# Kernel optimization log

Hardware: AMD Instinct MI355X
Metric: run time of the kernel (lower is better)

Reference implementation:

```python
import jax, jax.numpy as jnp
import numpy as np

N, L, H, E, FE = 32, 128, 16, 256, 4  # batch, seq_len, heads, embed_size, forward_expansion
EPS = 1e-5
NEG_SLOPE = 0.01


def _mask_positions(qe):
    # zero entries where j < L-1-i (torch: triu(ones,1).flip(1) == 1)
    Ld = qe.shape[-1]
    i = jnp.arange(Ld)[:, None]
    j = jnp.arange(Ld)[None, :]
    return jnp.where(j >= (Ld - 1 - i), qe, jnp.zeros((), qe.dtype))


def _skew(qe):
    # pad last dim on the left, reinterpret, drop first row -> relative skew
    n, h, Ld, _ = qe.shape
    p = jnp.pad(qe, ((0, 0), (0, 0), (0, 0), (1, 0)))
    return p.reshape(n, h, Ld + 1, Ld)[:, :, 1:, :]


def _batchnorm(x, gamma, beta):
    # BatchNorm1d(C=L*H) over (N, C, E): normalize over batch and embed dims
    mean = jnp.mean(x, axis=(0, 2), keepdims=True)
    var = jnp.var(x, axis=(0, 2), keepdims=True)
    return (x - mean) * jax.lax.rsqrt(var + EPS) * gamma[None, :, None] + beta[None, :, None]


def _leaky(x):
    return jnp.where(x >= 0, x, NEG_SLOPE * x)


def setup_inputs() -> dict:
    key = jax.random.key(0)
    ks = jax.random.split(key, 16)
    s_e = 1.0 / np.sqrt(E)
    d = {
        "x": jax.random.normal(ks[0], (N, L * H, E, 1), dtype=jnp.float32),
        "Wq": jax.random.normal(ks[1], (E, E), dtype=jnp.float32) * s_e,
        "bq": jnp.zeros((E,), jnp.float32),
        "Wk": jax.random.normal(ks[2], (E, E), dtype=jnp.float32) * s_e,
        "bk": jnp.zeros((E,), jnp.float32),
        "Wv": jax.random.normal(ks[3], (E, E), dtype=jnp.float32) * s_e,
        "bv": jnp.zeros((E,), jnp.float32),
        "Erel": jax.random.normal(ks[4], (H, L, E), dtype=jnp.float32),
        "Wo": jax.random.normal(ks[5], (E, E), dtype=jnp.float32) * s_e,
        "bo": jnp.zeros((E,), jnp.float32),
        "g1": jnp.ones((L * H,), jnp.float32),
        "be1": jnp.zeros((L * H,), jnp.float32),
        "g2": jnp.ones((L * H,), jnp.float32),
        "be2": jnp.zeros((L * H,), jnp.float32),
        "W1": jax.random.normal(ks[6], (E, FE * E), dtype=jnp.float32) * s_e,
        "b1": jnp.zeros((FE * E,), jnp.float32),
        "W2": jax.random.normal(ks[7], (FE * E, E), dtype=jnp.float32) * (1.0 / np.sqrt(FE * E)),
        "b2": jnp.zeros((E,), jnp.float32),
        "Wenc": jax.random.normal(ks[8], (E, E), dtype=jnp.float32) * s_e,
        "benc": jnp.zeros((E,), jnp.float32),
    }
    return d


def reference(x, Wq, bq, Wk, bk, Wv, bv, Erel, Wo, bo, g1, be1, g2, be2, W1, b1, W2, b2, Wenc, benc):
    xs = x[:, :, :, 0]  # (N, L*H, E)
    q = (xs @ Wq + bq).reshape(N, L, H, E)
    k = (xs @ Wk + bk).reshape(N, L, H, E)
    v = (xs @ Wv + bv).reshape(N, L, H, E)
    # relative-position skew term (Music-Transformer style)
    QE = jnp.einsum('nlhe,hme->nhlm', q, Erel)       # (N,H,L,L)
    S = _skew(_mask_positions(QE))                   # (N,H,L,L)
    qk = jnp.einsum('nqhe,nkhe->nhqk', q, k)         # (N,H,L,L)
    att = jax.nn.softmax(qk / jnp.sqrt(jnp.float32(E)), axis=-1) + S
    z = jnp.einsum('nhql,nlhe->nqhe', att, v).reshape(N, L * H, E)
    z = z @ Wo + bo
    h1 = _batchnorm(z + xs, g1, be1)
    ff = _leaky(h1 @ W1 + b1) @ W2 + b2
    out = _batchnorm(ff + h1, g2, be2)
    return out @ Wenc + benc
```

## Files before the change

kernel.cpp:

```cpp
#include <hip/hip_runtime.h>
#include <hip/hip_bf16.h>

using u16 = unsigned short;
typedef __attribute__((ext_vector_type(8))) short bf16x8;
typedef __attribute__((ext_vector_type(4))) float f32x4;

static constexpr float EPS_ = 1e-5f;
static constexpr float NEG_ = 0.01f;

__device__ __forceinline__ float bf2f(u16 u) { return __uint_as_float(((unsigned)u) << 16); }
__device__ __forceinline__ u16 f2bf(float f) {
    union { __hip_bfloat16 h; u16 u; } c; c.h = __float2bfloat16(f); return c.u;
}

#define MFMA16(a, b, c) __builtin_amdgcn_mfma_f32_16x16x32_bf16(a, b, c, 0, 0, 0)

__device__ __forceinline__ void gload16(const u16* g, u16* l) {
    __builtin_amdgcn_global_load_lds(
        (__attribute__((address_space(1))) void*)(u16*)g,
        (__attribute__((address_space(3))) void*)l, 16, 0, 0);
}

__device__ __forceinline__ void zero_acc(f32x4 acc[4][4]) {
    #pragma unroll
    for (int i = 0; i < 4; i++)
        #pragma unroll
        for (int j = 0; j < 4; j++)
            acc[i][j] = (f32x4){0.f, 0.f, 0.f, 0.f};
}

__device__ __forceinline__ int xswz(int nwg) {
    const int b = blockIdx.x;
    return (b & 7) * (nwg >> 3) + (b >> 3);
}

__device__ __forceinline__ void lds_core(
    const u16* __restrict__ Ag, int lda,
    const u16* __restrict__ Bg, int ldb, int K,
    u16* As, u16* Bs, f32x4 acc[4][4])
{
    const int tid = threadIdx.x;
    const int w = tid >> 6, lane = tid & 63;
    const int g = lane >> 4, r = lane & 15;
    const int wm = (w >> 1) * 64, wn = (w & 1) * 64;

    for (int kt = 0; kt < K; kt += 64) {
        #pragma unroll
        for (int j = 0; j < 4; j++) {
            const int ubase = (w * 4 + j) * 64;
            const int u = ubase + lane;
            const int row = u >> 3, cb = (u & 7) * 8;
            gload16(Ag + (size_t)row * lda + kt + cb, As + ubase * 8);
            gload16(Bg + (size_t)row * ldb + kt + cb, Bs + ubase * 8);
        }
        __syncthreads();
        #pragma unroll
        for (int kk = 0; kk < 2; kk++) {
            bf16x8 af[4], bfr[4];
            #pragma unroll
            for (int f = 0; f < 4; f++) {
                af[f]  = *(const bf16x8*)(As + (wm + f * 16 + r) * 64 + kk * 32 + g * 8);
                bfr[f] = *(const bf16x8*)(Bs + (wn + f * 16 + r) * 64 + kk * 32 + g * 8);
            }
            #pragma unroll
            for (int i = 0; i < 4; i++)
                #pragma unroll
                for (int j = 0; j < 4; j++)
                    acc[i][j] = MFMA16(af[i], bfr[j], acc[i][j]);
        }
        __syncthreads();
    }
}

template<int EPI, bool VTRANS, typename OutF, typename ResF>
__device__ __forceinline__ void epi_store(
    u16* Cs, f32x4 (&acc)[4][4], const float* biasBase, float scale,
    OutF outp, ResF resp)
{
    const int tid = threadIdx.x;
    const int w = tid >> 6, lane = tid & 63;
    const int g = lane >> 4, r = lane & 15;
    const int mb = (w >> 1) * 64, nb = (w & 1) * 64;

    #pragma unroll
    for (int fn = 0; fn < 4; fn++) {
        const int col = nb + fn * 16 + r;
        const float bv = biasBase ? biasBase[col] : 0.f;
        #pragma unroll
        for (int fm = 0; fm < 4; fm++) {
            #pragma unroll
            for (int reg = 0; reg < 4; reg++) {
                const int row = mb + fm * 16 + g * 4 + reg;
                float v = acc[fm][fn][reg] * scale + bv;
                if (EPI == 1) v = v >= 0.f ? v : NEG_ * v;
                int R, C;
                if (VTRANS) { R = col; C = ((row & 15) << 3) | (row >> 4); }
                else        { R = row; C = col; }
                Cs[R * 136 + C] = f2bf(v);
            }
        }
    }
    __syncthreads();
    #pragma unroll
    for (int p = 0; p < 8; p++) {
        const int ck = p * 256 + tid;
        const int row = ck >> 4, cc = ck & 15;
        bf16x8 v = *(const bf16x8*)(Cs + row * 136 + cc * 8);
        if constexpr (EPI == 3) {
            const bf16x8 rv = *(const bf16x8*)resp(row, cc);
            #pragma unroll
            for (int j = 0; j < 8; j++)
                v[j] = (short)f2bf(bf2f((u16)v[j]) + bf2f((u16)rv[j]));
        }
        *(bf16x8*)outp(row, cc) = v;
    }
}

__global__ __launch_bounds__(256) void cvt_k(const float* __restrict__ in,
                                             u16* __restrict__ out) {
    const size_t i8 = ((size_t)blockIdx.x * 256 + threadIdx.x) * 8;
    const float4 lo = *(const float4*)(in + i8);
    const float4 hi = *(const float4*)(in + i8 + 4);
    ushort4 o0, o1;
    o0.x = f2bf(lo.x); o0.y = f2bf(lo.y); o0.z = f2bf(lo.z); o0.w = f2bf(lo.w);
    o1.x = f2bf(hi.x); o1.y = f2bf(hi.y); o1.z = f2bf(hi.z); o1.w = f2bf(hi.w);
    *(ushort4*)(out + i8) = o0;
    *(ushort4*)(out + i8 + 4) = o1;
}

__global__ __launch_bounds__(256) void prep_w_k(
    const float* __restrict__ Wq, const float* __restrict__ Wk,
    const float* __restrict__ Wv, const float* __restrict__ Wo,
    const float* __restrict__ Wenc, const float* __restrict__ W1,
    const float* __restrict__ W2, const float* __restrict__ Erel,
    u16* __restrict__ Wqkvt, u16* __restrict__ Wot, u16* __restrict__ Wenct,
    u16* __restrict__ W1t, u16* __restrict__ W2t, u16* __restrict__ Erelb)
{
    const int bid = blockIdx.x, tid = threadIdx.x;
    if (bid < 1280) {
        const int jb = bid >> 8;
        const int t = ((bid & 255) << 8) | tid;
        const int n = t >> 8, k = t & 255;
        const float* src = jb == 0 ? Wq : jb == 1 ? Wk : jb == 2 ? Wv
                         : jb == 3 ? Wo : Wenc;
        const u16 v = f2bf(src[(k << 8) + n]);
        if (jb < 3)       Wqkvt[jb * 65536 + t] = v;
        else if (jb == 3) Wot[t] = v;
        else              Wenct[t] = v;
    } else if (bid < 2304) {
        const int t = ((bid - 1280) << 8) | tid;
        const int n = t >> 8, k = t & 255;
        W1t[t] = f2bf(W1[(k << 10) + n]);
    } else if (bid < 3328) {
        const int t = ((bid - 2304) << 8) | tid;
        const int n = t >> 10, k = t & 1023;
        W2t[t] = f2bf(W2[(k << 8) + n]);
    } else {
        const int t = ((bid - 3328) << 8) | tid;
        Erelb[t] = f2bf(Erel[t]);
    }
}

__global__ __launch_bounds__(256) void qkv_k(
    const u16* __restrict__ xbf, const u16* __restrict__ Wqkvt,
    const float* __restrict__ bq, const float* __restrict__ bk,
    const float* __restrict__ bv,
    u16* __restrict__ qo, u16* __restrict__ ko, u16* __restrict__ vo)
{
    __shared__ __align__(16) u16 SH[17408];
    u16* As = SH; u16* Bs = SH + 8192;
    const int f = xswz(3072);
    const int nblk = f % 6, mblk = f / 6;
    const int m0 = mblk * 128, n0 = nblk * 128;
    const int which = n0 >> 8;
    const float* bias = which == 0 ? bq : (which == 1 ? bk : bv);
    const int e0 = n0 & 255;

    f32x4 acc[4][4]; zero_acc(acc);
    lds_core(xbf + (size_t)m0 * 256, 256, Wqkvt + (size_t)n0 * 256, 256, 256,
             As, Bs, acc);

    const int nn = m0 >> 11, l0 = (m0 & 2047) >> 4;
    auto dummy = [&](int, int) -> const u16* { return nullptr; };
    if (which == 2) {
        epi_store<0, true>(SH, acc, bias + e0, 1.f,
            [&](int row, int cc) -> u16* {
                return vo + ((size_t)(nn * 16 + cc) * 256 + e0 + row) * 128 + l0;
            }, dummy);
    } else {
        u16* out = which == 0 ? qo : ko;
        epi_store<0, false>(SH, acc, bias + e0, 1.f,
            [&](int row, int cc) -> u16* {
                const int m = m0 + row;
                const int l = (m & 2047) >> 4, hh = m & 15;
                return out + ((size_t)(nn * 16 + hh) * 128 + l) * 256 + e0 + cc * 8;
            }, dummy);
    }
}

__global__ __launch_bounds__(256) void qkqe_k(
    const u16* __restrict__ q, const u16* __restrict__ kc,
    const u16* __restrict__ erel, u16* __restrict__ out)
{
    __shared__ __align__(16) u16 SH[17408];
    u16* As = SH; u16* Bs = SH + 8192;
    const int f = xswz(1024);
    const int b = f >> 1, h = b & 15;
    const int n0 = (f & 1) * 128;
    const u16* Ag = q + (size_t)b * 128 * 256;
    const u16* Bg = (n0 == 0) ? (kc + (size_t)b * 128 * 256)
                              : (erel + (size_t)h * 128 * 256);

    f32x4 acc[4][4]; zero_acc(acc);
    lds_core(Ag, 256, Bg, 256, 256, As, Bs, acc);

    const float scale = (n0 == 0) ? 0.0625f : 1.0f;
    auto dummy = [&](int, int) -> const u16* { return nullptr; };
    epi_store<0, false>(SH, acc, nullptr, scale,
        [&](int row, int cc) -> u16* {
            return out + ((size_t)b * 128 + row) * 256 + n0 + cc * 8;
        }, dummy);
}

__global__ __launch_bounds__(256) void softmax_k(
    const u16* __restrict__ qk, u16* __restrict__ att)
{
    const int r = blockIdx.x * 4 + (threadIdx.x >> 6);
    const int lane = threadIdx.x & 63;
    const int i = r & 127;
    const u16* row = qk + (size_t)r * 256;
    const float x0 = bf2f(row[lane]), x1 = bf2f(row[lane + 64]);
    float mx = fmaxf(x0, x1);
    #pragma unroll
    for (int o = 32; o; o >>= 1) mx = fmaxf(mx, __shfl_xor(mx, o));
    const float e0 = __expf(x0 - mx), e1 = __expf(x1 - mx);
    float s = e0 + e1;
    #pragma unroll
    for (int o = 32; o; o >>= 1) s += __shfl_xor(s, o);
    const float rinv = 1.0f / s;
    const float s0 = (lane <= i) ? bf2f(row[128 + 127 - i + lane]) : 0.f;
    const float s1 = (lane + 64 <= i) ? bf2f(row[128 + 127 - i + lane + 64]) : 0.f;
    att[(size_t)r * 128 + lane] = f2bf(e0 * rinv + s0);
    att[(size_t)r * 128 + lane + 64] = f2bf(e1 * rinv + s1);
}

__global__ __launch_bounds__(256) void av_k(
    const u16* __restrict__ att, const u16* __restrict__ vT,
    u16* __restrict__ zc)
{
    __shared__ __align__(16) u16 SH[17408];
    u16* As = SH; u16* Bs = SH + 8192;
    const int f = xswz(1024);
    const int b = f >> 1;
    const int n0 = (f & 1) * 128;
    const u16* Ag = att + (size_t)b * 128 * 128;
    const u16* Bg = vT + (size_t)b * 256 * 128 + (size_t)n0 * 128;

    f32x4 acc[4][4]; zero_acc(acc);
    lds_core(Ag, 128, Bg, 128, 128, As, Bs, acc);

    const int nn = b >> 4, hh = b & 15;
    auto dummy = [&](int, int) -> const u16* { return nullptr; };
    epi_store<0, false>(SH, acc, nullptr, 1.f,
        [&](int row, int cc) -> u16* {
            return zc + ((size_t)(nn * 2048 + row * 16 + hh)) * 256 + n0 + cc * 8;
        }, dummy);
}

template<int K, int Nn, int EPI, typename TO>
__global__ __launch_bounds__(256) void gemm_k(
    const u16* __restrict__ A, const u16* __restrict__ Wt,
    const float* __restrict__ bias, const u16* __restrict__ res,
    TO* __restrict__ out)
{
    __shared__ __align__(16) u16 SH[17408];
    u16* As = SH; u16* Bs = SH + 8192;
    constexpr int NB = Nn / 128;
    const int f = xswz(512 * NB);
    const int m0 = (f / NB) * 128, n0 = (f % NB) * 128;

    f32x4 acc[4][4]; zero_acc(acc);
    lds_core(A + (size_t)m0 * K, K, Wt + (size_t)n0 * K, K, K, As, Bs, acc);

    if constexpr (sizeof(TO) == 2) {
        epi_store<EPI, false>(SH, acc, bias + n0, 1.f,
            [&](int row, int cc) -> u16* {
                return ((u16*)out) + (size_t)(m0 + row) * Nn + n0 + cc * 8;
            },
            [&](int row, int cc) -> const u16* {
                return res + (size_t)(m0 + row) * Nn + n0 + cc * 8;
            });
    } else {
        const int tid = threadIdx.x;
        const int w = tid >> 6, lane = tid & 63;
        const int g = lane >> 4, r = lane & 15;
        const int mb = m0 + (w >> 1) * 64, nb = n0 + (w & 1) * 64;
        #pragma unroll
        for (int fn = 0; fn < 4; fn++) {
            const int n = nb + fn * 16 + r;
            const float bv4 = bias[n];
            #pragma unroll
            for (int fm = 0; fm < 4; fm++) {
                #pragma unroll
                for (int reg = 0; reg < 4; reg++) {
                    const int m = mb + fm * 16 + g * 4 + reg;
                    ((float*)out)[(size_t)m * Nn + n] = acc[fm][fn][reg] + bv4;
                }
            }
        }
    }
}

__global__ __launch_bounds__(256) void bnstats_k(
    const u16* __restrict__ x, const float* __restrict__ g,
    const float* __restrict__ be, float2* __restrict__ params)
{
    const int c = blockIdx.x, tid = threadIdx.x;
    float s = 0.f, s2 = 0.f;
    #pragma unroll 4
    for (int n = 0; n < 32; n++) {
        const float v = bf2f(x[((size_t)n * 2048 + c) * 256 + tid]);
        s += v; s2 += v * v;
    }
    #pragma unroll
    for (int o = 32; o; o >>= 1) { s += __shfl_xor(s, o); s2 += __shfl_xor(s2, o); }
    __shared__ float rs[4], rs2[4];
    const int w = tid >> 6;
    if ((tid & 63) == 0) { rs[w] = s; rs2[w] = s2; }
    __syncthreads();
    if (tid == 0) {
        s  = rs[0] + rs[1] + rs[2] + rs[3];
        s2 = rs2[0] + rs2[1] + rs2[2] + rs2[3];
        const float mean = s / 8192.f;
        const float var = s2 / 8192.f - mean * mean;
        const float a = g[c] * rsqrtf(var + EPS_);
        params[c] = make_float2(a, be[c] - mean * a);
    }
}

__global__ __launch_bounds__(256) void bnapply_k(
    const u16* __restrict__ in, const float2* __restrict__ p,
    u16* __restrict__ out)
{
    const size_t idx = (size_t)blockIdx.x * 256 + threadIdx.x;
    const int c = (int)((idx >> 5) & 2047);
    const float2 pp = p[c];
    const ushort4 v0 = ((const ushort4*)(in + idx * 8))[0];
    const ushort4 v1 = ((const ushort4*)(in + idx * 8))[1];
    ushort4 o0, o1;
    o0.x = f2bf(bf2f(v0.x) * pp.x + pp.y);
    o0.y = f2bf(bf2f(v0.y) * pp.x + pp.y);
    o0.z = f2bf(bf2f(v0.z) * pp.x + pp.y);
    o0.w = f2bf(bf2f(v0.w) * pp.x + pp.y);
    o1.x = f2bf(bf2f(v1.x) * pp.x + pp.y);
    o1.y = f2bf(bf2f(v1.y) * pp.x + pp.y);
    o1.z = f2bf(bf2f(v1.z) * pp.x + pp.y);
    o1.w = f2bf(bf2f(v1.w) * pp.x + pp.y);
    ((ushort4*)(out + idx * 8))[0] = o0;
    ((ushort4*)(out + idx * 8))[1] = o1;
}

extern "C" void kernel_launch(void* const* d_in, const int* in_sizes, int n_in,
                              void* d_out, int out_size, void* d_ws, size_t ws_size,
                              hipStream_t stream)
{
    const float* x    = (const float*)d_in[0];
    const float* Wq   = (const float*)d_in[1];
    const float* bq   = (const float*)d_in[2];
    const float* Wk   = (const float*)d_in[3];
    const float* bk   = (const float*)d_in[4];
    const float* Wv   = (const float*)d_in[5];
    const float* bv   = (const float*)d_in[6];
    const float* Erel = (const float*)d_in[7];
    const float* Wo   = (const float*)d_in[8];
    const float* bo   = (const float*)d_in[9];
    const float* g1   = (const float*)d_in[10];
    const float* be1  = (const float*)d_in[11];
    const float* g2   = (const float*)d_in[12];
    const float* be2  = (const float*)d_in[13];
    const float* W1   = (const float*)d_in[14];
    const float* b1   = (const float*)d_in[15];
    const float* W2   = (const float*)d_in[16];
    const float* b2   = (const float*)d_in[17];
    const float* Wenc = (const float*)d_in[18];
    const float* benc = (const float*)d_in[19];

    char* ws = (char*)d_ws;
    const size_t MB = 1ull << 20;
    const size_t KB = 1024;
    u16* xbf   = (u16*)(ws + 0 * MB);
    u16* h2n   = (u16*)(ws + 0 * MB);
    u16* qb    = (u16*)(ws + 32 * MB);
    u16* h1n   = (u16*)(ws + 32 * MB);
    u16* kb    = (u16*)(ws + 64 * MB);
    u16* vT    = (u16*)(ws + 96 * MB);
    u16* qkb   = (u16*)(ws + 128 * MB);
    u16* attb  = (u16*)(ws + 160 * MB);
    u16* ff1   = (u16*)(ws + 64 * MB);
    u16* zc    = (u16*)(ws + 176 * MB);
    u16* h1pre = (u16*)(ws + 208 * MB);
    u16* h2pre = (u16*)(ws + 208 * MB);
    u16* Wqkvt = (u16*)(ws + 240 * MB);
    u16* Wot   = (u16*)(ws + 240 * MB + 512 * KB);
    u16* Wenct = (u16*)(ws + 240 * MB + 640 * KB);
    u16* W1t   = (u16*)(ws + 240 * MB + 768 * KB);
    u16* W2t   = (u16*)(ws + 240 * MB + 1280 * KB);
    u16* Erelb = (u16*)(ws + 240 * MB + 1792 * KB);
    float2* p1 = (float2*)(ws + 243 * MB);
    float2* p2 = (float2*)(ws + 243 * MB + 16 * KB);

    const dim3 blk(256);

    cvt_k<<<dim3(8192), blk, 0, stream>>>(x, xbf);
    prep_w_k<<<dim3(5376), blk, 0, stream>>>(Wq, Wk, Wv, Wo, Wenc, W1, W2, Erel,
                                             Wqkvt, Wot, Wenct, W1t, W2t, Erelb);

    qkv_k<<<dim3(3072), blk, 0, stream>>>(xbf, Wqkvt, bq, bk, bv, qb, kb, vT);
    qkqe_k<<<dim3(1024), blk, 0, stream>>>(qb, kb, Erelb, qkb);
    softmax_k<<<dim3(16384), blk, 0, stream>>>(qkb, attb);
    av_k<<<dim3(1024), blk, 0, stream>>>(attb, vT, zc);
    gemm_k<256, 256, 3, u16><<<dim3(1024), blk, 0, stream>>>(
        zc, Wot, bo, xbf, h1pre);

    bnstats_k<<<dim3(2048), blk, 0, stream>>>(h1pre, g1, be1, p1);
    bnapply_k<<<dim3(8192), blk, 0, stream>>>(h1pre, p1, h1n);

    gemm_k<256, 1024, 1, u16><<<dim3(4096), blk, 0, stream>>>(
        h1n, W1t, b1, nullptr, ff1);
    gemm_k<1024, 256, 3, u16><<<dim3(1024), blk, 0, stream>>>(
        ff1, W2t, b2, h1n, h2pre);

    bnstats_k<<<dim3(2048), blk, 0, stream>>>(h2pre, g2, be2, p2);
    bnapply_k<<<dim3(8192), blk, 0, stream>>>(h2pre, p2, h2n);
    gemm_k<256, 256, 0, float><<<dim3(1024), blk, 0, stream>>>(
        h2n, Wenct, benc, nullptr, (float*)d_out);
}
```

Before: 328.3 us.

## Use 256x256 double-buffered GEMMs and fold batchnorm apply into following GEMMs

```diff
diff --git a/kernel.cpp b/kernel.cpp
--- a/kernel.cpp
+++ b/kernel.cpp
@@ -21,17 +21,256 @@
         (__attribute__((address_space(3))) void*)l, 16, 0, 0);
 }
 
-__device__ __forceinline__ void zero_acc(f32x4 acc[4][4]) {
-    #pragma unroll
-    for (int i = 0; i < 4; i++)
-        #pragma unroll
-        for (int j = 0; j < 4; j++)
-            acc[i][j] = (f32x4){0.f, 0.f, 0.f, 0.f};
-}
-
 __device__ __forceinline__ int xswz(int nwg) {
     const int b = blockIdx.x;
     return (b & 7) * (nwg >> 3) + (b >> 3);
+}
+
+template<int K>
+__device__ __forceinline__ void core256(
+    const u16* __restrict__ Ag, int lda,
+    const u16* __restrict__ Bg, int ldb,
+    u16* SH, f32x4 acc[8][4])
+{
+    const int tid = threadIdx.x;
+    const int w = tid >> 6, lane = tid & 63;
+    const int g = lane >> 4, r = lane & 15;
+    const int wr = w >> 2, wc = w & 3;
+    const int sx = r & 7;
+    constexpr int NT = K / 64;
+
+    #pragma unroll
+    for (int i = 0; i < 8; i++)
+        #pragma unroll
+        for (int j = 0; j < 4; j++)
+            acc[i][j] = (f32x4){0.f, 0.f, 0.f, 0.f};
+
+    auto stage = [&](int d, int kt, int rnd) {
+        const int j = rnd & 3;
+        const int u = j * 512 + w * 64 + lane;
+        const int row = u >> 3;
+        const int c8 = (u & 7) ^ (row & 7);
+        u16* ldst = SH + d * 32768 + (rnd < 4 ? 0 : 16384) + (j * 512 + w * 64) * 8;
+        const u16* src = (rnd < 4 ? Ag + (size_t)row * lda : Bg + (size_t)row * ldb)
+                         + kt + c8 * 8;
+        gload16(src, ldst);
+    };
+
+    #pragma unroll
+    for (int rnd = 0; rnd < 8; ++rnd) stage(0, 0, rnd);
+    asm volatile("s_waitcnt vmcnt(0)" ::: "memory");
+    __builtin_amdgcn_s_barrier();
+    __builtin_amdgcn_sched_barrier(0);
+
+    for (int t = 0; t < NT; ++t) {
+        const int d = t & 1;
+        const u16* Asd = SH + d * 32768;
+        const u16* Bsd = Asd + 16384;
+        #pragma unroll
+        for (int q = 0; q < 4; ++q) {
+            const int mh = q >> 1, nh = q & 1;
+            if (t + 1 < NT) {
+                stage(d ^ 1, (t + 1) * 64, q * 2);
+                stage(d ^ 1, (t + 1) * 64, q * 2 + 1);
+            }
+            bf16x8 af[2][4], bfr[2][2];
+            #pragma unroll
+            for (int kk = 0; kk < 2; ++kk) {
+                const int co = ((kk * 4 + g) ^ sx) * 8;
+                #pragma unroll
+                for (int f = 0; f < 4; ++f)
+                    af[kk][f] = *(const bf16x8*)(Asd + (wr*128 + mh*64 + f*16 + r) * 64 + co);
+                #pragma unroll
+                for (int e = 0; e < 2; ++e)
+                    bfr[kk][e] = *(const bf16x8*)(Bsd + (wc*64 + (nh*2+e)*16 + r) * 64 + co);
+            }
+            __builtin_amdgcn_s_setprio(1);
+            #pragma unroll
+            for (int kk = 0; kk < 2; ++kk)
+                #pragma unroll
+                for (int f = 0; f < 4; ++f)
+                    #pragma unroll
+                    for (int e = 0; e < 2; ++e)
+                        acc[mh*4+f][nh*2+e] =
+                            MFMA16(af[kk][f], bfr[kk][e], acc[mh*4+f][nh*2+e]);
+            __builtin_amdgcn_s_setprio(0);
+            if (q == 3) asm volatile("s_waitcnt vmcnt(0)" ::: "memory");
+            __builtin_amdgcn_s_barrier();
+            __builtin_amdgcn_sched_barrier(0);
+        }
+    }
+}
+
+template<int K, int NN, int MODE>
+__global__ __launch_bounds__(512, 2) void gemm256_k(
+    const u16* __restrict__ A, const u16* __restrict__ Bt,
+    const float* __restrict__ bias, const u16* __restrict__ res,
+    const float2* __restrict__ rp, const float* __restrict__ cs,
+    void* __restrict__ outv)
+{
+    __shared__ __align__(16) u16 SH[65536];
+    constexpr int NB = NN / 256;
+    const int f = xswz(256 * NB);
+    const int m0 = (f / NB) * 256, n0 = (f % NB) * 256;
+
+    f32x4 acc[8][4];
+    core256<K>(A + (size_t)m0 * K, K, Bt + (size_t)n0 * K, K, SH, acc);
+
+    const int tid = threadIdx.x;
+    const int w = tid >> 6, lane = tid & 63;
+    const int g = lane >> 4, r = lane & 15;
+    const int wr = w >> 2, wc = w & 3;
+
+    if constexpr (MODE == 3) {
+        float* out = (float*)outv;
+        #pragma unroll
+        for (int fn = 0; fn < 4; ++fn) {
+            const int n = n0 + wc * 64 + fn * 16 + r;
+            const float bv = bias[n], cv = cs[n];
+            #pragma unroll
+            for (int fm = 0; fm < 8; ++fm)
+                #pragma unroll
+                for (int reg = 0; reg < 4; ++reg) {
+                    const int m = m0 + wr * 128 + fm * 16 + g * 4 + reg;
+                    const float2 pp = rp[m & 2047];
+                    out[(size_t)m * NN + n] = pp.x * acc[fm][fn][reg] + pp.y * cv + bv;
+                }
+        }
+        return;
+    }
+    u16* out = (u16*)outv;
+    #pragma unroll
+    for (int h = 0; h < 2; ++h) {
+        if (wr == h) {
+            #pragma unroll
+            for (int fm = 0; fm < 8; ++fm)
+                #pragma unroll
+                for (int fn = 0; fn < 4; ++fn) {
+                    const int col = wc * 64 + fn * 16 + r;
+                    const float bv = bias[n0 + col];
+                    #pragma unroll
+                    for (int reg = 0; reg < 4; ++reg) {
+                        const int rl = fm * 16 + g * 4 + reg;
+                        float v = acc[fm][fn][reg];
+                        if constexpr (MODE == 1) {
+                            const float2 pp = rp[(m0 + h * 128 + rl) & 2047];
+                            v = pp.x * v + pp.y * cs[n0 + col] + bv;
+                            v = v >= 0.f ? v : NEG_ * v;
+                        } else {
+                            v += bv;
+                        }
+                        SH[rl * 264 + col] = f2bf(v);
+                    }
+                }
+        }
+        __builtin_amdgcn_s_barrier();
+        #pragma unroll
+        for (int p = 0; p < 8; ++p) {
+            const int ck = p * 512 + tid;
+            const int rl = ck >> 5, cc = ck & 31;
+            const int m = m0 + h * 128 + rl;
+            bf16x8 v = *(const bf16x8*)(SH + rl * 264 + cc * 8);
+            if constexpr (MODE == 0) {
+                const bf16x8 rv = *(const bf16x8*)(res + (size_t)m * NN + n0 + cc * 8);
+                #pragma unroll
+                for (int j = 0; j < 8; ++j)
+                    v[j] = (short)f2bf(bf2f((u16)v[j]) + bf2f((u16)rv[j]));
+            }
+            if constexpr (MODE == 2) {
+                const float2 pp = rp[m & 2047];
+                const bf16x8 rv = *(const bf16x8*)(res + (size_t)m * NN + n0 + cc * 8);
+                #pragma unroll
+                for (int j = 0; j < 8; ++j)
+                    v[j] = (short)f2bf(bf2f((u16)v[j]) + pp.x * bf2f((u16)rv[j]) + pp.y);
+            }
+            *(bf16x8*)(out + (size_t)m * NN + n0 + cc * 8) = v;
+        }
+        __builtin_amdgcn_s_barrier();
+    }
+}
+
+__global__ __launch_bounds__(512, 2) void qkv256_k(
+    const u16* __restrict__ xbf, const u16* __restrict__ Wqkvt,
+    const float* __restrict__ bq, const float* __restrict__ bk,
+    const float* __restrict__ bv,
+    u16* __restrict__ qo, u16* __restrict__ ko, u16* __restrict__ vo)
+{
+    __shared__ __align__(16) u16 SH[65536];
+    const int f = xswz(768);
+    const int m0 = (f / 3) * 256;
+    const int which = f % 3;
+    const float* bias = which == 0 ? bq : (which == 1 ? bk : bv);
+
+    f32x4 acc[8][4];
+    core256<256>(xbf + (size_t)m0 * 256, 256,
+                 Wqkvt + (size_t)which * 65536, 256, SH, acc);
+
+    const int tid = threadIdx.x;
+    const int w = tid >> 6, lane = tid & 63;
+    const int g = lane >> 4, r = lane & 15;
+    const int wr = w >> 2, wc = w & 3;
+    const int nn = m0 >> 11;
+
+    if (which < 2) {
+        u16* out = which == 0 ? qo : ko;
+        #pragma unroll
+        for (int h = 0; h < 2; ++h) {
+            if (wr == h) {
+                #pragma unroll
+                for (int fm = 0; fm < 8; ++fm)
+                    #pragma unroll
+                    for (int fn = 0; fn < 4; ++fn) {
+                        const int col = wc * 64 + fn * 16 + r;
+                        const float bv4 = bias[col];
+                        #pragma unroll
+                        for (int reg = 0; reg < 4; ++reg) {
+                            const int rl = fm * 16 + g * 4 + reg;
+                            SH[rl * 264 + col] = f2bf(acc[fm][fn][reg] + bv4);
+                        }
+                    }
+            }
+            __builtin_amdgcn_s_barrier();
+            #pragma unroll
+            for (int p = 0; p < 8; ++p) {
+                const int ck = p * 512 + tid;
+                const int rl = ck >> 5, cc = ck & 31;
+                const int m = m0 + h * 128 + rl;
+                const int l = (m & 2047) >> 4, hh = m & 15;
+                const bf16x8 v = *(const bf16x8*)(SH + rl * 264 + cc * 8);
+                *(bf16x8*)(out + ((size_t)(nn * 16 + hh) * 128 + l) * 256 + cc * 8) = v;
+            }
+            __builtin_amdgcn_s_barrier();
+        }
+    } else {
+        #pragma unroll
+        for (int h = 0; h < 2; ++h) {
+            if (wr == h) {
+                #pragma unroll
+                for (int fm = 0; fm < 8; ++fm)
+                    #pragma unroll
+                    for (int fn = 0; fn < 4; ++fn) {
+                        const int col = wc * 64 + fn * 16 + r;
+                        const float bv4 = bias[col];
+                        #pragma unroll
+                        for (int reg = 0; reg < 4; ++reg) {
+                            const int rl = fm * 16 + g * 4 + reg;
+                            SH[col * 136 + ((rl & 15) * 8 | (rl >> 4))] =
+                                f2bf(acc[fm][fn][reg] + bv4);
+                        }
+                    }
+            }
+            __builtin_amdgcn_s_barrier();
+            const int l0 = ((m0 + h * 128) & 2047) >> 4;
+            #pragma unroll
+            for (int p = 0; p < 8; ++p) {
+                const int ck = p * 512 + tid;
+                const int e = ck >> 4, hh = ck & 15;
+                const bf16x8 v = *(const bf16x8*)(SH + e * 136 + hh * 8);
+                *(bf16x8*)(vo + ((size_t)(nn * 16 + hh) * 256 + e) * 128 + l0) = v;
+            }
+            __builtin_amdgcn_s_barrier();
+        }
+    }
 }
 
 __device__ __forceinline__ void lds_core(
@@ -72,10 +311,9 @@
     }
 }
 
-template<int EPI, bool VTRANS, typename OutF, typename ResF>
-__device__ __forceinline__ void epi_store(
-    u16* Cs, f32x4 (&acc)[4][4], const float* biasBase, float scale,
-    OutF outp, ResF resp)
+template<typename OutF>
+__device__ __forceinline__ void epi_store128(
+    u16* Cs, f32x4 (&acc)[4][4], float scale, OutF outp)
 {
     const int tid = threadIdx.x;
     const int w = tid >> 6, lane = tid & 63;
@@ -85,35 +323,97 @@
     #pragma unroll
     for (int fn = 0; fn < 4; fn++) {
         const int col = nb + fn * 16 + r;
-        const float bv = biasBase ? biasBase[col] : 0.f;
-        #pragma unroll
-        for (int fm = 0; fm < 4; fm++) {
+        #pragma unroll
+        for (int fm = 0; fm < 4; fm++)
             #pragma unroll
             for (int reg = 0; reg < 4; reg++) {
                 const int row = mb + fm * 16 + g * 4 + reg;
-                float v = acc[fm][fn][reg] * scale + bv;
-                if (EPI == 1) v = v >= 0.f ? v : NEG_ * v;
-                int R, C;
-                if (VTRANS) { R = col; C = ((row & 15) << 3) | (row >> 4); }
-                else        { R = row; C = col; }
-                Cs[R * 136 + C] = f2bf(v);
-            }
-        }
+                Cs[row * 136 + col] = f2bf(acc[fm][fn][reg] * scale);
+            }
     }
     __syncthreads();
     #pragma unroll
     for (int p = 0; p < 8; p++) {
         const int ck = p * 256 + tid;
         const int row = ck >> 4, cc = ck & 15;
-        bf16x8 v = *(const bf16x8*)(Cs + row * 136 + cc * 8);
-        if constexpr (EPI == 3) {
-            const bf16x8 rv = *(const bf16x8*)resp(row, cc);
-            #pragma unroll
-            for (int j = 0; j < 8; j++)
-                v[j] = (short)f2bf(bf2f((u16)v[j]) + bf2f((u16)rv[j]));
-        }
+        const bf16x8 v = *(const bf16x8*)(Cs + row * 136 + cc * 8);
         *(bf16x8*)outp(row, cc) = v;
     }
+}
+
+__global__ __launch_bounds__(256) void qkqe_k(
+    const u16* __restrict__ q, const u16* __restrict__ kc,
+    const u16* __restrict__ erel, u16* __restrict__ out)
+{
+    __shared__ __align__(16) u16 SH[17408];
+    u16* As = SH; u16* Bs = SH + 8192;
+    const int f = xswz(1024);
+    const int b = f >> 1, h = b & 15;
+    const int n0 = (f & 1) * 128;
+    const u16* Ag = q + (size_t)b * 128 * 256;
+    const u16* Bg = (n0 == 0) ? (kc + (size_t)b * 128 * 256)
+                              : (erel + (size_t)h * 128 * 256);
+
+    f32x4 acc[4][4];
+    #pragma unroll
+    for (int i = 0; i < 4; i++)
+        #pragma unroll
+        for (int j = 0; j < 4; j++) acc[i][j] = (f32x4){0.f,0.f,0.f,0.f};
+    lds_core(Ag, 256, Bg, 256, 256, As, Bs, acc);
+
+    const float scale = (n0 == 0) ? 0.0625f : 1.0f;
+    epi_store128(SH, acc, scale,
+        [&](int row, int cc) -> u16* {
+            return out + ((size_t)b * 128 + row) * 256 + n0 + cc * 8;
+        });
+}
+
+__global__ __launch_bounds__(256) void softmax_k(
+    const u16* __restrict__ qk, u16* __restrict__ att)
+{
+    const int r = blockIdx.x * 4 + (threadIdx.x >> 6);
+    const int lane = threadIdx.x & 63;
+    const int i = r & 127;
+    const u16* row = qk + (size_t)r * 256;
+    const float x0 = bf2f(row[lane]), x1 = bf2f(row[lane + 64]);
+    float mx = fmaxf(x0, x1);
+    #pragma unroll
+    for (int o = 32; o; o >>= 1) mx = fmaxf(mx, __shfl_xor(mx, o));
+    const float e0 = __expf(x0 - mx), e1 = __expf(x1 - mx);
+    float s = e0 + e1;
+    #pragma unroll
+    for (int o = 32; o; o >>= 1) s += __shfl_xor(s, o);
+    const float rinv = 1.0f / s;
+    const float s0 = (lane <= i) ? bf2f(row[128 + 127 - i + lane]) : 0.f;
+    const float s1 = (lane + 64 <= i) ? bf2f(row[128 + 127 - i + lane + 64]) : 0.f;
+    att[(size_t)r * 128 + lane] = f2bf(e0 * rinv + s0);
+    att[(size_t)r * 128 + lane + 64] = f2bf(e1 * rinv + s1);
+}
+
+__global__ __launch_bounds__(256) void av_k(
+    const u16* __restrict__ att, const u16* __restrict__ vT,
+    u16* __restrict__ zc)
+{
+    __shared__ __align__(16) u16 SH[17408];
+    u16* As = SH; u16* Bs = SH + 8192;
+    const int f = xswz(1024);
+    const int b = f >> 1;
+    const int n0 = (f & 1) * 128;
+    const u16* Ag = att + (size_t)b * 128 * 128;
+    const u16* Bg = vT + (size_t)b * 256 * 128 + (size_t)n0 * 128;
+
+    f32x4 acc[4][4];
+    #pragma unroll
+    for (int i = 0; i < 4; i++)
+        #pragma unroll
+        for (int j = 0; j < 4; j++) acc[i][j] = (f32x4){0.f,0.f,0.f,0.f};
+    lds_core(Ag, 128, Bg, 128, 128, As, Bs, acc);
+
+    const int nn = b >> 4, hh = b & 15;
+    epi_store128(SH, acc, 1.f,
+        [&](int row, int cc) -> u16* {
+            return zc + ((size_t)(nn * 2048 + row * 16 + hh)) * 256 + n0 + cc * 8;
+        });
 }
 
 __global__ __launch_bounds__(256) void cvt_k(const float* __restrict__ in,
@@ -134,7 +434,8 @@
     const float* __restrict__ Wenc, const float* __restrict__ W1,
     const float* __restrict__ W2, const float* __restrict__ Erel,
     u16* __restrict__ Wqkvt, u16* __restrict__ Wot, u16* __restrict__ Wenct,
-    u16* __restrict__ W1t, u16* __restrict__ W2t, u16* __restrict__ Erelb)
+    u16* __restrict__ W1t, u16* __restrict__ W2t, u16* __restrict__ Erelb,
+    float* __restrict__ cs1, float* __restrict__ csE)
 {
     const int bid = blockIdx.x, tid = threadIdx.x;
     if (bid < 1280) {
@@ -155,158 +456,20 @@
         const int t = ((bid - 2304) << 8) | tid;
         const int n = t >> 10, k = t & 1023;
         W2t[t] = f2bf(W2[(k << 8) + n]);
-    } else {
+    } else if (bid < 5376) {
         const int t = ((bid - 3328) << 8) | tid;
         Erelb[t] = f2bf(Erel[t]);
-    }
-}
-
-__global__ __launch_bounds__(256) void qkv_k(
-    const u16* __restrict__ xbf, const u16* __restrict__ Wqkvt,
-    const float* __restrict__ bq, const float* __restrict__ bk,
-    const float* __restrict__ bv,
-    u16* __restrict__ qo, u16* __restrict__ ko, u16* __restrict__ vo)
-{
-    __shared__ __align__(16) u16 SH[17408];
-    u16* As = SH; u16* Bs = SH + 8192;
-    const int f = xswz(3072);
-    const int nblk = f % 6, mblk = f / 6;
-    const int m0 = mblk * 128, n0 = nblk * 128;
-    const int which = n0 >> 8;
-    const float* bias = which == 0 ? bq : (which == 1 ? bk : bv);
-    const int e0 = n0 & 255;
-
-    f32x4 acc[4][4]; zero_acc(acc);
-    lds_core(xbf + (size_t)m0 * 256, 256, Wqkvt + (size_t)n0 * 256, 256, 256,
-             As, Bs, acc);
-
-    const int nn = m0 >> 11, l0 = (m0 & 2047) >> 4;
-    auto dummy = [&](int, int) -> const u16* { return nullptr; };
-    if (which == 2) {
-        epi_store<0, true>(SH, acc, bias + e0, 1.f,
-            [&](int row, int cc) -> u16* {
-                return vo + ((size_t)(nn * 16 + cc) * 256 + e0 + row) * 128 + l0;
-            }, dummy);
     } else {
-        u16* out = which == 0 ? qo : ko;
-        epi_store<0, false>(SH, acc, bias + e0, 1.f,
-            [&](int row, int cc) -> u16* {
-                const int m = m0 + row;
-                const int l = (m & 2047) >> 4, hh = m & 15;
-                return out + ((size_t)(nn * 16 + hh) * 128 + l) * 256 + e0 + cc * 8;
-            }, dummy);
-    }
-}
-
-__global__ __launch_bounds__(256) void qkqe_k(
-    const u16* __restrict__ q, const u16* __restrict__ kc,
-    const u16* __restrict__ erel, u16* __restrict__ out)
-{
-    __shared__ __align__(16) u16 SH[17408];
-    u16* As = SH; u16* Bs = SH + 8192;
-    const int f = xswz(1024);
-    const int b = f >> 1, h = b & 15;
-    const int n0 = (f & 1) * 128;
-    const u16* Ag = q + (size_t)b * 128 * 256;
-    const u16* Bg = (n0 == 0) ? (kc + (size_t)b * 128 * 256)
-                              : (erel + (size_t)h * 128 * 256);
-
-    f32x4 acc[4][4]; zero_acc(acc);
-    lds_core(Ag, 256, Bg, 256, 256, As, Bs, acc);
-
-    const float scale = (n0 == 0) ? 0.0625f : 1.0f;
-    auto dummy = [&](int, int) -> const u16* { return nullptr; };
-    epi_store<0, false>(SH, acc, nullptr, scale,
-        [&](int row, int cc) -> u16* {
-            return out + ((size_t)b * 128 + row) * 256 + n0 + cc * 8;
-        }, dummy);
-}
-
-__global__ __launch_bounds__(256) void softmax_k(
-    const u16* __restrict__ qk, u16* __restrict__ att)
-{
-    const int r = blockIdx.x * 4 + (threadIdx.x >> 6);
-    const int lane = threadIdx.x & 63;
-    const int i = r & 127;
-    const u16* row = qk + (size_t)r * 256;
-    const float x0 = bf2f(row[lane]), x1 = bf2f(row[lane + 64]);
-    float mx = fmaxf(x0, x1);
-    #pragma unroll
-    for (int o = 32; o; o >>= 1) mx = fmaxf(mx, __shfl_xor(mx, o));
-    const float e0 = __expf(x0 - mx), e1 = __expf(x1 - mx);
-    float s = e0 + e1;
-    #pragma unroll
-    for (int o = 32; o; o >>= 1) s += __shfl_xor(s, o);
-    const float rinv = 1.0f / s;
-    const float s0 = (lane <= i) ? bf2f(row[128 + 127 - i + lane]) : 0.f;
-    const float s1 = (lane + 64 <= i) ? bf2f(row[128 + 127 - i + lane + 64]) : 0.f;
-    att[(size_t)r * 128 + lane] = f2bf(e0 * rinv + s0);
-    att[(size_t)r * 128 + lane + 64] = f2bf(e1 * rinv + s1);
-}
-
-__global__ __launch_bounds__(256) void av_k(
-    const u16* __restrict__ att, const u16* __restrict__ vT,
-    u16* __restrict__ zc)
-{
-    __shared__ __align__(16) u16 SH[17408];
-    u16* As = SH; u16* Bs = SH + 8192;
-    const int f = xswz(1024);
-    const int b = f >> 1;
-    const int n0 = (f & 1) * 128;
-    const u16* Ag = att + (size_t)b * 128 * 128;
-    const u16* Bg = vT + (size_t)b * 256 * 128 + (size_t)n0 * 128;
-
-    f32x4 acc[4][4]; zero_acc(acc);
-    lds_core(Ag, 128, Bg, 128, 128, As, Bs, acc);
-
-    const int nn = b >> 4, hh = b & 15;
-    auto dummy = [&](int, int) -> const u16* { return nullptr; };
-    epi_store<0, false>(SH, acc, nullptr, 1.f,
-        [&](int row, int cc) -> u16* {
-            return zc + ((size_t)(nn * 2048 + row * 16 + hh)) * 256 + n0 + cc * 8;
-        }, dummy);
-}
-
-template<int K, int Nn, int EPI, typename TO>
-__global__ __launch_bounds__(256) void gemm_k(
-    const u16* __restrict__ A, const u16* __restrict__ Wt,
-    const float* __restrict__ bias, const u16* __restrict__ res,
-    TO* __restrict__ out)
-{
-    __shared__ __align__(16) u16 SH[17408];
-    u16* As = SH; u16* Bs = SH + 8192;
-    constexpr int NB = Nn / 128;
-    const int f = xswz(512 * NB);
-    const int m0 = (f / NB) * 128, n0 = (f % NB) * 128;
-
-    f32x4 acc[4][4]; zero_acc(acc);
-    lds_core(A + (size_t)m0 * K, K, Wt + (size_t)n0 * K, K, K, As, Bs, acc);
-
-    if constexpr (sizeof(TO) == 2) {
-        epi_store<EPI, false>(SH, acc, bias + n0, 1.f,
-            [&](int row, int cc) -> u16* {
-                return ((u16*)out) + (size_t)(m0 + row) * Nn + n0 + cc * 8;
-            },
-            [&](int row, int cc) -> const u16* {
-                return res + (size_t)(m0 + row) * Nn + n0 + cc * 8;
-            });
-    } else {
-        const int tid = threadIdx.x;
-        const int w = tid >> 6, lane = tid & 63;
-        const int g = lane >> 4, r = lane & 15;
-        const int mb = m0 + (w >> 1) * 64, nb = n0 + (w & 1) * 64;
-        #pragma unroll
-        for (int fn = 0; fn < 4; fn++) {
-            const int n = nb + fn * 16 + r;
-            const float bv4 = bias[n];
-            #pragma unroll
-            for (int fm = 0; fm < 4; fm++) {
-                #pragma unroll
-                for (int reg = 0; reg < 4; reg++) {
-                    const int m = mb + fm * 16 + g * 4 + reg;
-                    ((float*)out)[(size_t)m * Nn + n] = acc[fm][fn][reg] + bv4;
-                }
-            }
+        const int n = (bid - 5376) * 256 + tid;
+        if (n < 1024) {
+            float s = 0.f;
+            for (int k = 0; k < 256; ++k) s += bf2f(f2bf(W1[(size_t)k * 1024 + n]));
+            cs1[n] = s;
+        } else {
+            const int n2 = n - 1024;
+            float s = 0.f;
+            for (int k = 0; k < 256; ++k) s += bf2f(f2bf(Wenc[(size_t)k * 256 + n2]));
+            csE[n2] = s;
         }
     }
 }
@@ -336,28 +499,6 @@
         const float a = g[c] * rsqrtf(var + EPS_);
         params[c] = make_float2(a, be[c] - mean * a);
     }
-}
-
-__global__ __launch_bounds__(256) void bnapply_k(
-    const u16* __restrict__ in, const float2* __restrict__ p,
-    u16* __restrict__ out)
-{
-    const size_t idx = (size_t)blockIdx.x * 256 + threadIdx.x;
-    const int c = (int)((idx >> 5) & 2047);
-    const float2 pp = p[c];
-    const ushort4 v0 = ((const ushort4*)(in + idx * 8))[0];
-    const ushort4 v1 = ((const ushort4*)(in + idx * 8))[1];
-    ushort4 o0, o1;
-    o0.x = f2bf(bf2f(v0.x) * pp.x + pp.y);
-    o0.y = f2bf(bf2f(v0.y) * pp.x + pp.y);
-    o0.z = f2bf(bf2f(v0.z) * pp.x + pp.y);
-    o0.w = f2bf(bf2f(v0.w) * pp.x + pp.y);
-    o1.x = f2bf(bf2f(v1.x) * pp.x + pp.y);
-    o1.y = f2bf(bf2f(v1.y) * pp.x + pp.y);
-    o1.z = f2bf(bf2f(v1.z) * pp.x + pp.y);
-    o1.w = f2bf(bf2f(v1.w) * pp.x + pp.y);
-    ((ushort4*)(out + idx * 8))[0] = o0;
-    ((ushort4*)(out + idx * 8))[1] = o1;
 }
 
 extern "C" void kernel_launch(void* const* d_in, const int* in_sizes, int n_in,
@@ -389,9 +530,8 @@
     const size_t MB = 1ull << 20;
     const size_t KB = 1024;
     u16* xbf   = (u16*)(ws + 0 * MB);
-    u16* h2n   = (u16*)(ws + 0 * MB);
+    u16* h2pre = (u16*)(ws + 32 * MB);
     u16* qb    = (u16*)(ws + 32 * MB);
-    u16* h1n   = (u16*)(ws + 32 * MB);
     u16* kb    = (u16*)(ws + 64 * MB);
     u16* vT    = (u16*)(ws + 96 * MB);
     u16* qkb   = (u16*)(ws + 128 * MB);
@@ -399,7 +539,6 @@
     u16* ff1   = (u16*)(ws + 64 * MB);
     u16* zc    = (u16*)(ws + 176 * MB);
     u16* h1pre = (u16*)(ws + 208 * MB);
-    u16* h2pre = (u16*)(ws + 208 * MB);
     u16* Wqkvt = (u16*)(ws + 240 * MB);
     u16* Wot   = (u16*)(ws + 240 * MB + 512 * KB);
     u16* Wenct = (u16*)(ws + 240 * MB + 640 * KB);
@@ -408,30 +547,31 @@
     u16* Erelb = (u16*)(ws + 240 * MB + 1792 * KB);
     float2* p1 = (float2*)(ws + 243 * MB);
     float2* p2 = (float2*)(ws + 243 * MB + 16 * KB);
-
-    const dim3 blk(256);
-
-    cvt_k<<<dim3(8192), blk, 0, stream>>>(x, xbf);
-    prep_w_k<<<dim3(5376), blk, 0, stream>>>(Wq, Wk, Wv, Wo, Wenc, W1, W2, Erel,
-                                             Wqkvt, Wot, Wenct, W1t, W2t, Erelb);
-
-    qkv_k<<<dim3(3072), blk, 0, stream>>>(xbf, Wqkvt, bq, bk, bv, qb, kb, vT);
-    qkqe_k<<<dim3(1024), blk, 0, stream>>>(qb, kb, Erelb, qkb);
-    softmax_k<<<dim3(16384), blk, 0, stream>>>(qkb, attb);
-    av_k<<<dim3(1024), blk, 0, stream>>>(attb, vT, zc);
-    gemm_k<256, 256, 3, u16><<<dim3(1024), blk, 0, stream>>>(
-        zc, Wot, bo, xbf, h1pre);
-
-    bnstats_k<<<dim3(2048), blk, 0, stream>>>(h1pre, g1, be1, p1);
-    bnapply_k<<<dim3(8192), blk, 0, stream>>>(h1pre, p1, h1n);
-
-    gemm_k<256, 1024, 1, u16><<<dim3(4096), blk, 0, stream>>>(
-        h1n, W1t, b1, nullptr, ff1);
-    gemm_k<1024, 256, 3, u16><<<dim3(1024), blk, 0, stream>>>(
-        ff1, W2t, b2, h1n, h2pre);
-
-    bnstats_k<<<dim3(2048), blk, 0, stream>>>(h2pre, g2, be2, p2);
-    bnapply_k<<<dim3(8192), blk, 0, stream>>>(h2pre, p2, h2n);
-    gemm_k<256, 256, 0, float><<<dim3(1024), blk, 0, stream>>>(
-        h2n, Wenct, benc, nullptr, (float*)d_out);
-}
+    float* cs1 = (float*)(ws + 243 * MB + 32 * KB);
+    float* csE = (float*)(ws + 243 * MB + 40 * KB);
+
+    const dim3 b256(256), b512(512);
+
+    cvt_k<<<dim3(8192), b256, 0, stream>>>(x, xbf);
+    prep_w_k<<<dim3(5381), b256, 0, stream>>>(Wq, Wk, Wv, Wo, Wenc, W1, W2, Erel,
+                                              Wqkvt, Wot, Wenct, W1t, W2t, Erelb,
+                                              cs1, csE);
+
+    qkv256_k<<<dim3(768), b512, 0, stream>>>(xbf, Wqkvt, bq, bk, bv, qb, kb, vT);
+    qkqe_k<<<dim3(1024), b256, 0, stream>>>(qb, kb, Erelb, qkb);
+    softmax_k<<<dim3(16384), b256, 0, stream>>>(qkb, attb);
+    av_k<<<dim3(1024), b256, 0, stream>>>(attb, vT, zc);
+    gemm256_k<256, 256, 0><<<dim3(256), b512, 0, stream>>>(
+        zc, Wot, bo, xbf, nullptr, nullptr, h1pre);
+
+    bnstats_k<<<dim3(2048), b256, 0, stream>>>(h1pre, g1, be1, p1);
+
+    gemm256_k<256, 1024, 1><<<dim3(1024), b512, 0, stream>>>(
+        h1pre, W1t, b1, nullptr, p1, cs1, ff1);
+    gemm256_k<1024, 256, 2><<<dim3(256), b512, 0, stream>>>(
+        ff1, W2t, b2, h1pre, p1, nullptr, h2pre);
+
+    bnstats_k<<<dim3(2048), b256, 0, stream>>>(h2pre, g2, be2, p2);
+    gemm256_k<256, 256, 3><<<dim3(256), b512, 0, stream>>>(
+        h2pre, Wenct, benc, nullptr, p2, csE, (float*)d_out);
+}
```

Measured after the change: 357.3 us. +8.8%, slower.
